# Performance work log

Hardware: AMD Instinct MI355X
Metric: run time of the kernel (lower is better)

The kernel has to match this reference:

```python
import jax, jax.numpy as jnp
import numpy as np

DIM = 192
HEADS = 4
B, H, W = 4, 128, 128


def _dwconv3(x, w):
    # depthwise 3x3, padding=1: w has shape [C, 1, 3, 3], groups = C
    return jax.lax.conv_general_dilated(
        x, w, window_strides=(1, 1), padding='SAME',
        feature_group_count=x.shape[1],
        dimension_numbers=('NCHW', 'OIHW', 'NCHW'))


def _conv1x1(x, w):
    # w: [O, C] (squeezed 1x1 kernel), bias=False
    return jnp.einsum('bchw,oc->bohw', x, w)


def _l2norm(t):
    # torch F.normalize(dim=-1), eps=1e-12
    n = jnp.sqrt(jnp.sum(t * t, axis=-1, keepdims=True))
    return t / jnp.maximum(n, 1e-12)


def setup_inputs() -> dict:
    key = jax.random.key(0)
    ks = jax.random.split(key, 12)
    s = 0.05
    return {
        'x': jax.random.normal(ks[0], (B, DIM, H, W), jnp.float32),
        'x_hidden': jax.random.normal(ks[1], (B, DIM, H, W), jnp.float32),
        'qkv_w': jax.random.normal(ks[2], (3 * DIM, DIM), jnp.float32) * s,
        'qkv_dw_w': jax.random.normal(ks[3], (3 * DIM, 1, 3, 3), jnp.float32) * s,
        'q_mut_w': jax.random.normal(ks[4], (DIM, DIM), jnp.float32) * s,
        'q_mut_dw_w': jax.random.normal(ks[5], (DIM, 1, 3, 3), jnp.float32) * s,
        'kv_mut_w': jax.random.normal(ks[6], (2 * DIM, DIM), jnp.float32) * s,
        'kv_mut_dw_w': jax.random.normal(ks[7], (2 * DIM, 1, 3, 3), jnp.float32) * s,
        'proj_w': jax.random.normal(ks[8], (DIM, 2 * DIM), jnp.float32) * s,
        'temperature': jnp.ones((HEADS, 1, 1), jnp.float32),
        'temperature_mut': jnp.ones((HEADS, 1, 1), jnp.float32),
    }


def reference(x, x_hidden, qkv_w, qkv_dw_w, q_mut_w, q_mut_dw_w,
              kv_mut_w, kv_mut_dw_w, proj_w, temperature, temperature_mut):
    b, c, h, w = x.shape
    heads = HEADS

    qkv = _dwconv3(_conv1x1(x, qkv_w), qkv_dw_w)
    q, k, v = jnp.split(qkv, 3, axis=1)
    q_mut = _dwconv3(_conv1x1(x, q_mut_w), q_mut_dw_w)
    kv_mut = _dwconv3(_conv1x1(x_hidden, kv_mut_w), kv_mut_dw_w)
    k_mut, v_mut = jnp.split(kv_mut, 2, axis=1)

    def rs(t):  # b (head c') h w -> b head c' (h w)
        return t.reshape(b, heads, c // heads, h * w)

    q, k, v = rs(q), rs(k), rs(v)
    q_mut, k_mut, v_mut = rs(q_mut), rs(k_mut), rs(v_mut)

    q, k = _l2norm(q), _l2norm(k)
    q_mut, k_mut = _l2norm(q_mut), _l2norm(k_mut)

    # channel-wise (transposed) attention: [b, head, c', c']
    attn = jax.nn.softmax(
        jnp.einsum('bhcn,bhdn->bhcd', q, k) * temperature, axis=-1)
    cross = jax.nn.softmax(
        jnp.einsum('bhcn,bhdn->bhcd', q_mut, k_mut) * temperature_mut, axis=-1)

    out = jnp.einsum('bhcd,bhdn->bhcn', attn, v).reshape(b, c, h, w)
    out_mut = jnp.einsum('bhcd,bhdn->bhcn', cross, v_mut).reshape(b, c, h, w)

    return _conv1x1(jnp.concatenate((out, out_mut), axis=1), proj_w)
```

## Files before the change

kernel.cpp:

```cpp
#include <hip/hip_runtime.h>
#include <hip/hip_bf16.h>

typedef __hip_bfloat16 bf16;
using short8  = __attribute__((ext_vector_type(8))) short;
using float4_ = __attribute__((ext_vector_type(4))) float;

#define B_    4
#define C_    192
#define NN    16384
#define HEADS 4
#define CHD   48
#define TOT   1152

__device__ __forceinline__ float b2f(bf16 v) { return __bfloat162float(v); }
__device__ __forceinline__ float s2f(short s) {
    return __uint_as_float(((unsigned)(unsigned short)s) << 16);
}

__global__ __launch_bounds__(256) void kprep_w(
    const float* __restrict__ qkv_w, const float* __restrict__ qm_w,
    const float* __restrict__ kvm_w, bf16* __restrict__ Wb)
{
    int i = blockIdx.x * 256 + threadIdx.x;
    if (i >= TOT * C_) return;
    int r = i / C_, c = i % C_;
    float v = (r < 576) ? qkv_w[r * C_ + c]
            : (r < 768) ? qm_w[(r - 576) * C_ + c]
                        : kvm_w[(r - 768) * C_ + c];
    Wb[i] = __float2bfloat16(v);
}

__global__ __launch_bounds__(256) void kprep_x(
    const float* __restrict__ x, const float* __restrict__ xh,
    int b, bf16* __restrict__ Xt)
{
    const int src = blockIdx.z;
    const float* in = (src == 0 ? x : xh) + (size_t)b * C_ * NN;
    bf16* outp = Xt + (size_t)src * NN * C_;
    const int n0 = blockIdx.x * 32, c0 = blockIdx.y * 32;
    __shared__ float t[32][33];
    const int tid = threadIdx.x;
    const int ln = tid & 31, lc = tid >> 5;
    #pragma unroll
    for (int it = 0; it < 4; ++it)
        t[lc + it * 8][ln] = in[(size_t)(c0 + lc + it * 8) * NN + n0 + ln];
    __syncthreads();
    const int lc2 = tid & 31, ln2 = tid >> 5;
    #pragma unroll
    for (int it = 0; it < 4; ++it)
        outp[(size_t)(n0 + ln2 + it * 8) * C_ + c0 + lc2] =
            __float2bfloat16(t[lc2][ln2 + it * 8]);
}

__global__ __launch_bounds__(256) void kgemm(
    const bf16* __restrict__ Wb, const bf16* __restrict__ Xt,
    bf16* __restrict__ Y)
{
    const int nt0 = blockIdx.x * 128;
    const int mt0 = blockIdx.y * 64;
    const int tid = threadIdx.x;
    const bf16* Xs = Xt + (mt0 >= 768 ? (size_t)NN * C_ : 0);

    __shared__ short sA[64][72];
    __shared__ short sB[128][72];

    const int wave = tid >> 6, lane = tid & 63;
    const int mw = (wave & 1) * 32, nw = (wave >> 1) * 64;
    const int lm = lane & 15, lq = lane >> 4;

    float4_ acc[2][4];
    #pragma unroll
    for (int i = 0; i < 2; ++i)
        #pragma unroll
        for (int j = 0; j < 4; ++j)
            acc[i][j] = (float4_){0.f, 0.f, 0.f, 0.f};

    for (int kc = 0; kc < 192; kc += 64) {
        __syncthreads();
        {
            int r = tid >> 3, c8 = (tid & 7) * 8;
            #pragma unroll
            for (int it = 0; it < 2; ++it, r += 32)
                *(short8*)&sA[r][c8] =
                    *(const short8*)&Wb[(size_t)(mt0 + r) * C_ + kc + c8];
        }
        {
            int r = tid >> 3, c8 = (tid & 7) * 8;
            #pragma unroll
            for (int it = 0; it < 4; ++it, r += 32)
                *(short8*)&sB[r][c8] =
                    *(const short8*)&Xs[(size_t)(nt0 + r) * C_ + kc + c8];
        }
        __syncthreads();
        #pragma unroll
        for (int kk = 0; kk < 64; kk += 32) {
            short8 af[2], bfr[4];
            const int ko = kk + lq * 8;
            #pragma unroll
            for (int i = 0; i < 2; ++i)
                af[i] = *(const short8*)&sA[mw + i * 16 + lm][ko];
            #pragma unroll
            for (int j = 0; j < 4; ++j)
                bfr[j] = *(const short8*)&sB[nw + j * 16 + lm][ko];
            #pragma unroll
            for (int i = 0; i < 2; ++i)
                #pragma unroll
                for (int j = 0; j < 4; ++j)
                    acc[i][j] = __builtin_amdgcn_mfma_f32_16x16x32_bf16(
                        af[i], bfr[j], acc[i][j], 0, 0, 0);
        }
    }
    #pragma unroll
    for (int i = 0; i < 2; ++i)
        #pragma unroll
        for (int j = 0; j < 4; ++j) {
            const int n = nt0 + nw + j * 16 + lm;
            #pragma unroll
            for (int r = 0; r < 4; ++r) {
                const int m = mt0 + mw + i * 16 + lq * 4 + r;
                Y[(size_t)m * NN + n] = __float2bfloat16(acc[i][j][r]);
            }
        }
}

__device__ __forceinline__ void kdw_load_row(
    float* r, const bf16* __restrict__ Yc, int row, int x0)
{
    if (row < 0 || row > 127) {
        #pragma unroll
        for (int i = 0; i < 10; ++i) r[i] = 0.f;
        return;
    }
    const bf16* p = Yc + row * 128 + x0;
    short8 v = *(const short8*)p;
    #pragma unroll
    for (int i = 0; i < 8; ++i) r[i + 1] = s2f(v[i]);
    r[0] = (x0 > 0)   ? b2f(p[-1]) : 0.f;
    r[9] = (x0 < 120) ? b2f(p[8])  : 0.f;
}

__global__ __launch_bounds__(256) void kdw(
    const bf16* __restrict__ Y,
    const float* __restrict__ qkv_dw, const float* __restrict__ qm_dw,
    const float* __restrict__ kvm_dw, int b, bf16* __restrict__ QT,
    float* __restrict__ nrmsq)
{
    const int ch  = blockIdx.x;
    const int tid = threadIdx.x;
    const int tx = tid & 15, ty = tid >> 4;
    const int x0 = tx * 8;
    const int y0 = blockIdx.y * 64 + ty * 4;

    const float* dwp = (ch < 576) ? qkv_dw + (size_t)ch * 9
                     : (ch < 768) ? qm_dw + (size_t)(ch - 576) * 9
                                  : kvm_dw + (size_t)(ch - 768) * 9;
    float w[9];
    #pragma unroll
    for (int i = 0; i < 9; ++i) w[i] = dwp[i];

    const bf16* Yc = Y + (size_t)ch * NN;
    bf16* qout = QT + ((size_t)b * TOT + ch) * NN;

    float r0[10], r1[10], r2[10];
    kdw_load_row(r0, Yc, y0 - 1, x0);
    kdw_load_row(r1, Yc, y0,     x0);

    float ssq = 0.f;
    #pragma unroll
    for (int yy = 0; yy < 4; ++yy) {
        kdw_load_row(r2, Yc, y0 + yy + 1, x0);
        short8 sv;
        #pragma unroll
        for (int xx = 0; xx < 8; ++xx) {
            float s = w[0] * r0[xx] + w[1] * r0[xx + 1] + w[2] * r0[xx + 2]
                    + w[3] * r1[xx] + w[4] * r1[xx + 1] + w[5] * r1[xx + 2]
                    + w[6] * r2[xx] + w[7] * r2[xx + 1] + w[8] * r2[xx + 2];
            ssq += s * s;
            bf16 h = __float2bfloat16(s);
            sv[xx] = *reinterpret_cast<short*>(&h);
        }
        *(short8*)&qout[(size_t)(y0 + yy) * 128 + x0] = sv;
        #pragma unroll
        for (int i = 0; i < 10; ++i) { r0[i] = r1[i]; r1[i] = r2[i]; }
    }

    int cls = -1, ci = 0;
    if (ch < 192)                    { cls = 0; ci = ch; }
    else if (ch < 384)               { cls = 1; ci = ch - 192; }
    else if (ch >= 576 && ch < 768)  { cls = 2; ci = ch - 576; }
    else if (ch >= 768 && ch < 960)  { cls = 3; ci = ch - 768; }
    if (cls >= 0) {
        #pragma unroll
        for (int off = 32; off > 0; off >>= 1) ssq += __shfl_down(ssq, off);
        __shared__ float red[4];
        if ((tid & 63) == 0) red[tid >> 6] = ssq;
        __syncthreads();
        if (tid == 0)
            atomicAdd(&nrmsq[(b * 4 + cls) * 192 + ci],
                      red[0] + red[1] + red[2] + red[3]);
    }
}

__global__ __launch_bounds__(256) void ktv(
    const bf16* __restrict__ QT, bf16* __restrict__ Vt)
{
    const int bs = blockIdx.z;
    const int b = bs >> 1, src = bs & 1;
    const int n0 = blockIdx.x * 32, c0 = blockIdx.y * 32;
    const int chbase = (src == 0) ? 384 : 960;
    const int colbase = (src == 0) ? 0 : 192;
    __shared__ short t[32][33];
    const int tid = threadIdx.x;
    const int ln = tid & 31, lc = tid >> 5;
    const bf16* qb = QT + ((size_t)b * TOT + chbase + c0) * NN;
    #pragma unroll
    for (int it = 0; it < 4; ++it)
        t[lc + it * 8][ln] =
            *(const short*)&qb[(size_t)(lc + it * 8) * NN + n0 + ln];
    __syncthreads();
    const int lc2 = tid & 31, ln2 = tid >> 5;
    bf16* vb = Vt + (size_t)b * NN * 384;
    #pragma unroll
    for (int it = 0; it < 4; ++it)
        *(short*)&vb[(size_t)(n0 + ln2 + it * 8) * 384 + colbase + c0 + lc2] =
            t[lc2][ln2 + it * 8];
}

__global__ __launch_bounds__(256) void k3_mfma(
    const bf16* __restrict__ QT, float* __restrict__ Gpart)
{
    const int chunk = blockIdx.x;
    const int t = blockIdx.y >> 2, h = blockIdx.y & 3;
    const int b = blockIdx.z;
    const int qch = (t == 0 ? 0 : 576) + h * CHD;
    const int kch = (t == 0 ? 192 : 768) + h * CHD;
    const bf16* qp = QT + ((size_t)b * TOT + qch) * NN;
    const bf16* kp = QT + ((size_t)b * TOT + kch) * NN;

    const int tid = threadIdx.x;
    const int wave = tid >> 6, lane = tid & 63;
    const int lm = lane & 15, lq = lane >> 4;
    const int n0 = chunk * 512 + wave * 128;

    float4_ acc[3][3];
    #pragma unroll
    for (int i = 0; i < 3; ++i)
        #pragma unroll
        for (int j = 0; j < 3; ++j)
            acc[i][j] = (float4_){0.f, 0.f, 0.f, 0.f};

    #pragma unroll
    for (int kk = 0; kk < 128; kk += 32) {
        short8 af[3], bfr[3];
        const int ko = n0 + kk + lq * 8;
        #pragma unroll
        for (int i = 0; i < 3; ++i)
            af[i] = *(const short8*)&qp[(size_t)(i * 16 + lm) * NN + ko];
        #pragma unroll
        for (int j = 0; j < 3; ++j)
            bfr[j] = *(const short8*)&kp[(size_t)(j * 16 + lm) * NN + ko];
        #pragma unroll
        for (int i = 0; i < 3; ++i)
            #pragma unroll
            for (int j = 0; j < 3; ++j)
                acc[i][j] = __builtin_amdgcn_mfma_f32_16x16x32_bf16(
                    af[i], bfr[j], acc[i][j], 0, 0, 0);
    }

    __shared__ float sW[4][48 * 49];
    #pragma unroll
    for (int i = 0; i < 3; ++i)
        #pragma unroll
        for (int j = 0; j < 3; ++j)
            #pragma unroll
            for (int r = 0; r < 4; ++r)
                sW[wave][(i * 16 + lq * 4 + r) * 49 + j * 16 + lm] = acc[i][j][r];
    __syncthreads();

    const int gidx = ((t * 4 + b) * 4 + h);
    float* Gp = Gpart + ((size_t)gidx * 32 + chunk) * 2304;
    for (int idx = tid; idx < 2304; idx += 256) {
        const int c = idx / 48, d = idx % 48;
        Gp[idx] = sW[0][c * 49 + d] + sW[1][c * 49 + d]
                + sW[2][c * 49 + d] + sW[3][c * 49 + d];
    }
}

__global__ __launch_bounds__(256) void kred(
    const float* __restrict__ Gpart, float* __restrict__ G)
{
    const int idx = blockIdx.x * 256 + threadIdx.x;
    if (idx >= 32 * 2304) return;
    const int g = idx / 2304, i = idx % 2304;
    const float* p = Gpart + (size_t)g * 32 * 2304 + i;
    float s = 0.f;
    #pragma unroll
    for (int ch = 0; ch < 32; ++ch) s += p[(size_t)ch * 2304];
    G[(size_t)g * 2304 + i] = s;
}

__global__ __launch_bounds__(256) void k4a_softmax(
    const float* __restrict__ G, const float* __restrict__ nrmsq,
    const float* __restrict__ tq, const float* __restrict__ tm,
    float* __restrict__ P)
{
    const int gidx = blockIdx.x;
    const int h = gidx & 3, tb = gidx >> 2;
    const int b = tb & 3, t = tb >> 2;
    const float* Gp = G + (size_t)gidx * 2304;
    float* Pp = P + (size_t)gidx * 2304;

    const int tid = threadIdx.x;
    const int wave = tid >> 6, lane = tid & 63;
    const int clsq = (t == 0) ? 0 : 2, clsk = (t == 0) ? 1 : 3;
    const float tmp = (t == 0 ? tq[h] : tm[h]);

    float nk = 1.f;
    if (lane < 48)
        nk = fmaxf(sqrtf(fmaxf(nrmsq[(b * 4 + clsk) * 192 + h * 48 + lane], 0.f)),
                   1e-12f);
    const float sk = tmp / nk;

    const int c0 = blockIdx.y * 12 + wave * 3;
    #pragma unroll
    for (int cc = 0; cc < 3; ++cc) {
        const int c = c0 + cc;
        const float nq =
            fmaxf(sqrtf(fmaxf(nrmsq[(b * 4 + clsq) * 192 + h * 48 + c], 0.f)),
                  1e-12f);
        float L = -1e30f;
        if (lane < 48) L = Gp[c * 48 + lane] * sk / nq;
        float mx = L;
        #pragma unroll
        for (int off = 32; off > 0; off >>= 1)
            mx = fmaxf(mx, __shfl_xor(mx, off));
        float e = (lane < 48) ? expf(L - mx) : 0.f;
        float sum = e;
        #pragma unroll
        for (int off = 32; off > 0; off >>= 1)
            sum += __shfl_xor(sum, off);
        if (lane < 48) Pp[c * 48 + lane] = e / sum;
    }
}

__global__ __launch_bounds__(256) void k4b_fold(
    const float* __restrict__ P, const float* __restrict__ proj_w,
    bf16* __restrict__ Mb)
{
    const int gidx = blockIdx.x;
    const int h = gidx & 3, tb = gidx >> 2;
    const int b = tb & 3, t = tb >> 2;
    const int o0 = blockIdx.y * 48;
    const int colb = t * 192 + h * 48;

    __shared__ float sP[48][49];
    __shared__ float sW[48][49];
    const int tid = threadIdx.x;
    const float* Pp = P + (size_t)gidx * 2304;

    for (int idx = tid; idx < 2304; idx += 256) {
        const int r = idx / 48, q = idx % 48;
        sP[r][q] = Pp[idx];
        sW[r][q] = proj_w[(size_t)(o0 + r) * 384 + colb + q];
    }
    __syncthreads();

    for (int idx = tid; idx < 2304; idx += 256) {
        const int o = idx / 48, d = idx % 48;
        float s = 0.f;
        #pragma unroll
        for (int c = 0; c < 48; ++c) s += sW[o][c] * sP[c][d];
        Mb[((size_t)b * 192 + o0 + o) * 384 + colb + d] = __float2bfloat16(s);
    }
}

__global__ __launch_bounds__(256) void k5_mfma(
    const bf16* __restrict__ Mb, const bf16* __restrict__ Vt,
    float* __restrict__ out)
{
    const int nt0 = blockIdx.x * 128;
    const int mt0 = blockIdx.y * 64;
    const int b   = blockIdx.z;
    const int tid = threadIdx.x;

    __shared__ short sB[128][72];

    const int wave = tid >> 6, lane = tid & 63;
    const int mw = (wave & 1) * 32, nw = (wave >> 1) * 64;
    const int lm = lane & 15, lq = lane >> 4;

    const bf16* Vb = Vt + (size_t)b * NN * 384;
    const bf16* Mp = Mb + (size_t)b * 192 * 384;

    float4_ acc[2][4];
    #pragma unroll
    for (int i = 0; i < 2; ++i)
        #pragma unroll
        for (int j = 0; j < 4; ++j)
            acc[i][j] = (float4_){0.f, 0.f, 0.f, 0.f};

    for (int kc = 0; kc < 384; kc += 64) {
        __syncthreads();
        {
            int r = tid >> 3, c8 = (tid & 7) * 8;
            #pragma unroll
            for (int it = 0; it < 4; ++it, r += 32)
                *(short8*)&sB[r][c8] =
                    *(const short8*)&Vb[(size_t)(nt0 + r) * 384 + kc + c8];
        }
        __syncthreads();
        #pragma unroll
        for (int kk = 0; kk < 64; kk += 32) {
            short8 af[2], bfr[4];
            const int ko = kk + lq * 8;
            #pragma unroll
            for (int i = 0; i < 2; ++i)
                af[i] = *(const short8*)
                    &Mp[(size_t)(mt0 + mw + i * 16 + lm) * 384 + kc + ko];
            #pragma unroll
            for (int j = 0; j < 4; ++j)
                bfr[j] = *(const short8*)&sB[nw + j * 16 + lm][ko];
            #pragma unroll
            for (int i = 0; i < 2; ++i)
                #pragma unroll
                for (int j = 0; j < 4; ++j)
                    acc[i][j] = __builtin_amdgcn_mfma_f32_16x16x32_bf16(
                        af[i], bfr[j], acc[i][j], 0, 0, 0);
        }
    }
    #pragma unroll
    for (int i = 0; i < 2; ++i)
        #pragma unroll
        for (int j = 0; j < 4; ++j) {
            const int n = nt0 + nw + j * 16 + lm;
            #pragma unroll
            for (int r = 0; r < 4; ++r) {
                const int m = mt0 + mw + i * 16 + lq * 4 + r;
                out[((size_t)b * C_ + m) * NN + n] = acc[i][j][r];
            }
        }
}

extern "C" void kernel_launch(void* const* d_in, const int* in_sizes, int n_in,
                              void* d_out, int out_size, void* d_ws, size_t ws_size,
                              hipStream_t stream)
{
    const float* x     = (const float*)d_in[0];
    const float* xh    = (const float*)d_in[1];
    const float* qkvw  = (const float*)d_in[2];
    const float* qkvdw = (const float*)d_in[3];
    const float* qmw   = (const float*)d_in[4];
    const float* qmdw  = (const float*)d_in[5];
    const float* kvmw  = (const float*)d_in[6];
    const float* kvmdw = (const float*)d_in[7];
    const float* projw = (const float*)d_in[8];
    const float* tq    = (const float*)d_in[9];
    const float* tm    = (const float*)d_in[10];
    float* out = (float*)d_out;

    char* ws = (char*)d_ws;
    size_t off = 0;
    bf16*  QT = (bf16*)(ws + off);  off += (size_t)B_ * TOT * NN * 2;
    bf16*  Y  = (bf16*)(ws + off);
    bf16*  Vt = (bf16*)(ws + off);  off += (size_t)TOT * NN * 2;
    bf16*  Xt = (bf16*)(ws + off);  off += (size_t)2 * NN * C_ * 2;
    bf16*  Wb = (bf16*)(ws + off);  off += (size_t)TOT * C_ * 2;
    float* nrm = (float*)(ws + off); off += (size_t)B_ * 4 * 192 * 4;
    float* G   = (float*)(ws + off); off += (size_t)2 * B_ * HEADS * 48 * 48 * 4;
    bf16*  Mb  = (bf16*)(ws + off);  off += (size_t)B_ * 192 * 384 * 2;
    float* Gpart = (float*)(ws + off); off += (size_t)32 * 32 * 2304 * 4;
    float* P = Gpart;

    hipMemsetAsync(nrm, 0, (size_t)B_ * 4 * 192 * 4, stream);

    kprep_w<<<dim3((TOT * C_ + 255) / 256), 256, 0, stream>>>(qkvw, qmw, kvmw, Wb);

    for (int b = 0; b < B_; ++b) {
        kprep_x<<<dim3(512, 6, 2), 256, 0, stream>>>(x, xh, b, Xt);
        kgemm  <<<dim3(128, 18), 256, 0, stream>>>(Wb, Xt, Y);
        kdw    <<<dim3(1152, 2), 256, 0, stream>>>(Y, qkvdw, qmdw, kvmdw, b, QT, nrm);
    }

    ktv        <<<dim3(512, 6, 8), 256, 0, stream>>>(QT, Vt);
    k3_mfma    <<<dim3(32, 8, B_), 256, 0, stream>>>(QT, Gpart);
    kred       <<<dim3((32 * 2304 + 255) / 256), 256, 0, stream>>>(Gpart, G);
    k4a_softmax<<<dim3(32, 4), 256, 0, stream>>>(G, nrm, tq, tm, P);
    k4b_fold   <<<dim3(32, 4), 256, 0, stream>>>(P, projw, Mb);
    k5_mfma    <<<dim3(128, 3, B_), 256, 0, stream>>>(Mb, Vt, out);
}
```

Baseline: 399.9 us.

## Enlarge GEMM tiles to reuse staged X and V tiles across more output rows

The qkv projection GEMM now stages the whole 128x192 X tile in shared memory once and computes a 128x128 output tile per block, reading weights straight from global memory instead of staging them. The final projection GEMM covers all 192 output channels per block, so each V tile is loaded once instead of three times. The aim is to cut redundant global and LDS traffic and the number of barriers. In exchange, accumulator registers grow (up to 24 float4 per lane), which may lower occupancy, and the grids have fewer blocks.

```diff
diff --git a/kernel.cpp b/kernel.cpp
--- a/kernel.cpp
+++ b/kernel.cpp
@@ -57,67 +57,61 @@
     bf16* __restrict__ Y)
 {
     const int nt0 = blockIdx.x * 128;
-    const int mt0 = blockIdx.y * 64;
+    const int mt0 = blockIdx.y * 128;
     const int tid = threadIdx.x;
     const bf16* Xs = Xt + (mt0 >= 768 ? (size_t)NN * C_ : 0);
 
-    __shared__ short sA[64][72];
-    __shared__ short sB[128][72];
+    __shared__ short sB[128][200];
+
+    {
+        const short* src = (const short*)(Xs + (size_t)nt0 * C_);
+        #pragma unroll
+        for (int it = 0; it < 12; ++it) {
+            const int idx = it * 256 + tid;
+            const int r = idx / 24, g = (idx % 24) * 8;
+            *(short8*)&sB[r][g] = *(const short8*)&src[idx * 8];
+        }
+    }
+    __syncthreads();
 
     const int wave = tid >> 6, lane = tid & 63;
-    const int mw = (wave & 1) * 32, nw = (wave >> 1) * 64;
+    const int wm = (wave & 1) * 64, wn = (wave >> 1) * 64;
     const int lm = lane & 15, lq = lane >> 4;
 
-    float4_ acc[2][4];
-    #pragma unroll
-    for (int i = 0; i < 2; ++i)
+    float4_ acc[4][4];
+    #pragma unroll
+    for (int i = 0; i < 4; ++i)
         #pragma unroll
         for (int j = 0; j < 4; ++j)
             acc[i][j] = (float4_){0.f, 0.f, 0.f, 0.f};
 
-    for (int kc = 0; kc < 192; kc += 64) {
-        __syncthreads();
-        {
-            int r = tid >> 3, c8 = (tid & 7) * 8;
-            #pragma unroll
-            for (int it = 0; it < 2; ++it, r += 32)
-                *(short8*)&sA[r][c8] =
-                    *(const short8*)&Wb[(size_t)(mt0 + r) * C_ + kc + c8];
-        }
-        {
-            int r = tid >> 3, c8 = (tid & 7) * 8;
-            #pragma unroll
-            for (int it = 0; it < 4; ++it, r += 32)
-                *(short8*)&sB[r][c8] =
-                    *(const short8*)&Xs[(size_t)(nt0 + r) * C_ + kc + c8];
-        }
-        __syncthreads();
-        #pragma unroll
-        for (int kk = 0; kk < 64; kk += 32) {
-            short8 af[2], bfr[4];
-            const int ko = kk + lq * 8;
-            #pragma unroll
-            for (int i = 0; i < 2; ++i)
-                af[i] = *(const short8*)&sA[mw + i * 16 + lm][ko];
+    #pragma unroll
+    for (int kk = 0; kk < 192; kk += 32) {
+        short8 af[4], bfr[4];
+        const int ko = kk + lq * 8;
+        #pragma unroll
+        for (int i = 0; i < 4; ++i)
+            af[i] = *(const short8*)
+                &Wb[(size_t)(mt0 + wm + i * 16 + lm) * C_ + ko];
+        #pragma unroll
+        for (int j = 0; j < 4; ++j)
+            bfr[j] = *(const short8*)&sB[wn + j * 16 + lm][ko];
+        #pragma unroll
+        for (int i = 0; i < 4; ++i)
             #pragma unroll
             for (int j = 0; j < 4; ++j)
-                bfr[j] = *(const short8*)&sB[nw + j * 16 + lm][ko];
-            #pragma unroll
-            for (int i = 0; i < 2; ++i)
-                #pragma unroll
-                for (int j = 0; j < 4; ++j)
-                    acc[i][j] = __builtin_amdgcn_mfma_f32_16x16x32_bf16(
-                        af[i], bfr[j], acc[i][j], 0, 0, 0);
-        }
-    }
-    #pragma unroll
-    for (int i = 0; i < 2; ++i)
+                acc[i][j] = __builtin_amdgcn_mfma_f32_16x16x32_bf16(
+                    af[i], bfr[j], acc[i][j], 0, 0, 0);
+    }
+
+    #pragma unroll
+    for (int i = 0; i < 4; ++i)
         #pragma unroll
         for (int j = 0; j < 4; ++j) {
-            const int n = nt0 + nw + j * 16 + lm;
+            const int n = nt0 + wn + j * 16 + lm;
             #pragma unroll
             for (int r = 0; r < 4; ++r) {
-                const int m = mt0 + mw + i * 16 + lq * 4 + r;
+                const int m = mt0 + wm + i * 16 + lq * 4 + r;
                 Y[(size_t)m * NN + n] = __float2bfloat16(acc[i][j][r]);
             }
         }
@@ -379,22 +373,21 @@
     float* __restrict__ out)
 {
     const int nt0 = blockIdx.x * 128;
-    const int mt0 = blockIdx.y * 64;
     const int b   = blockIdx.z;
     const int tid = threadIdx.x;
 
     __shared__ short sB[128][72];
 
     const int wave = tid >> 6, lane = tid & 63;
-    const int mw = (wave & 1) * 32, nw = (wave >> 1) * 64;
+    const int wm = (wave & 1) * 96, wn = (wave >> 1) * 64;
     const int lm = lane & 15, lq = lane >> 4;
 
     const bf16* Vb = Vt + (size_t)b * NN * 384;
     const bf16* Mp = Mb + (size_t)b * 192 * 384;
 
-    float4_ acc[2][4];
-    #pragma unroll
-    for (int i = 0; i < 2; ++i)
+    float4_ acc[6][4];
+    #pragma unroll
+    for (int i = 0; i < 6; ++i)
         #pragma unroll
         for (int j = 0; j < 4; ++j)
             acc[i][j] = (float4_){0.f, 0.f, 0.f, 0.f};
@@ -411,17 +404,17 @@
         __syncthreads();
         #pragma unroll
         for (int kk = 0; kk < 64; kk += 32) {
-            short8 af[2], bfr[4];
+            short8 af[6], bfr[4];
             const int ko = kk + lq * 8;
             #pragma unroll
-            for (int i = 0; i < 2; ++i)
+            for (int i = 0; i < 6; ++i)
                 af[i] = *(const short8*)
-                    &Mp[(size_t)(mt0 + mw + i * 16 + lm) * 384 + kc + ko];
+                    &Mp[(size_t)(wm + i * 16 + lm) * 384 + kc + ko];
             #pragma unroll
             for (int j = 0; j < 4; ++j)
-                bfr[j] = *(const short8*)&sB[nw + j * 16 + lm][ko];
-            #pragma unroll
-            for (int i = 0; i < 2; ++i)
+                bfr[j] = *(const short8*)&sB[wn + j * 16 + lm][ko];
+            #pragma unroll
+            for (int i = 0; i < 6; ++i)
                 #pragma unroll
                 for (int j = 0; j < 4; ++j)
                     acc[i][j] = __builtin_amdgcn_mfma_f32_16x16x32_bf16(
@@ -429,13 +422,13 @@
         }
     }
     #pragma unroll
-    for (int i = 0; i < 2; ++i)
+    for (int i = 0; i < 6; ++i)
         #pragma unroll
         for (int j = 0; j < 4; ++j) {
-            const int n = nt0 + nw + j * 16 + lm;
+            const int n = nt0 + wn + j * 16 + lm;
             #pragma unroll
             for (int r = 0; r < 4; ++r) {
-                const int m = mt0 + mw + i * 16 + lq * 4 + r;
+                const int m = wm + i * 16 + lq * 4 + r;
                 out[((size_t)b * C_ + m) * NN + n] = acc[i][j][r];
             }
         }
@@ -477,7 +470,7 @@
 
     for (int b = 0; b < B_; ++b) {
         kprep_x<<<dim3(512, 6, 2), 256, 0, stream>>>(x, xh, b, Xt);
-        kgemm  <<<dim3(128, 18), 256, 0, stream>>>(Wb, Xt, Y);
+        kgemm  <<<dim3(128, 9), 256, 0, stream>>>(Wb, Xt, Y);
         kdw    <<<dim3(1152, 2), 256, 0, stream>>>(Y, qkvdw, qmdw, kvmdw, b, QT, nrm);
     }
 
@@ -486,5 +479,5 @@
     kred       <<<dim3((32 * 2304 + 255) / 256), 256, 0, stream>>>(Gpart, G);
     k4a_softmax<<<dim3(32, 4), 256, 0, stream>>>(G, nrm, tq, tm, P);
     k4b_fold   <<<dim3(32, 4), 256, 0, stream>>>(P, projw, Mb);
-    k5_mfma    <<<dim3(128, 3, B_), 256, 0, stream>>>(Mb, Vt, out);
-}
+    k5_mfma    <<<dim3(128, 1, B_), 256, 0, stream>>>(Mb, Vt, out);
+}
```

Result: slower. 433.2 us (+8.3%).
